# Kernel tuning notes

Measured on AMD Instinct MI355X. Metric: run time of the kernel, lower is better.

Reference implementation:

```python
import jax, jax.numpy as jnp
import numpy as np

B, D_IN, T = 16, 512, 4096
D_CB, K = 8, 1024
COMMITMENT = 1.0


def _weight_norm(v, g):
    # torch weight_norm with dim=0: w[o] = g[o] * v[o] / ||v[o]||
    return g[:, None] * v / jnp.sqrt(jnp.sum(v * v, axis=1, keepdims=True))


def setup_inputs() -> dict:
    key = jax.random.key(0)
    ks = jax.random.split(key, 8)
    return {
        "z": jax.random.normal(ks[0], (B, D_IN, T), dtype=jnp.float32),
        "in_v": jax.random.normal(ks[1], (D_CB, D_IN), dtype=jnp.float32) * 0.05,
        "in_g": jax.random.uniform(ks[2], (D_CB,), dtype=jnp.float32, minval=0.5, maxval=1.5),
        "in_b": jax.random.normal(ks[3], (D_CB,), dtype=jnp.float32) * 0.01,
        "out_v": jax.random.normal(ks[4], (D_IN, D_CB), dtype=jnp.float32) * 0.05,
        "out_g": jax.random.uniform(ks[5], (D_IN,), dtype=jnp.float32, minval=0.5, maxval=1.5),
        "out_b": jax.random.normal(ks[6], (D_IN,), dtype=jnp.float32) * 0.01,
        "codebook": jax.random.normal(ks[7], (K, D_CB), dtype=jnp.float32),
    }


def reference(z, in_v, in_g, in_b, out_v, out_g, out_b, codebook):
    z = z.astype(jnp.float32)
    # in_project: weight-normed 1x1 conv == per-timestep linear [D_IN -> D_CB]
    w_in = _weight_norm(in_v, in_g)                       # [D_CB, D_IN]
    z_e = jnp.einsum('cd,bdt->bct', w_in, z) + in_b[None, :, None]  # [B, D_CB, T]

    enc = jnp.transpose(z_e, (0, 2, 1))                   # [B, T, D_CB]
    cb = codebook.astype(jnp.float32)                     # [K, D_CB]
    # squared euclidean distance via expansion
    d = (jnp.sum(enc * enc, axis=-1, keepdims=True)
         - 2.0 * jnp.einsum('btd,kd->btk', enc, cb)
         + jnp.sum(cb * cb, axis=-1)[None, None, :])      # [B, T, K]
    indices = jnp.argmin(d, axis=-1)                      # [B, T] int

    z_q = jnp.transpose(cb[indices], (0, 2, 1))           # [B, D_CB, T]
    commit_loss = jnp.mean((z_e - jax.lax.stop_gradient(z_q)) ** 2, axis=(1, 2)) * COMMITMENT  # [B]

    # straight-through estimator
    z_q_st = z_e + jax.lax.stop_gradient(z_q - z_e)

    w_out = _weight_norm(out_v, out_g)                    # [D_IN, D_CB]
    out = jnp.einsum('cd,bdt->bct', w_out, z_q_st) + out_b[None, :, None]  # [B, D_IN, T]
    return out, commit_loss, indices
```

## Files before the change

### kernel.cpp

```cpp
#include <hip/hip_runtime.h>
#include <math.h>

#define NB 16
#define DIN 512
#define TT 4096
#define DCB 8
#define KC 1024
#define NW 8


__global__ __launch_bounds__(512) void vq_setup(
    const float* __restrict__ in_v, const float* __restrict__ in_g,
    const float* __restrict__ out_v, const float* __restrict__ out_g,
    const float* __restrict__ cb, float* __restrict__ ws)
{
    int tid = threadIdx.x;
    float* w_inT = ws;
    float* w_out = ws + 4096;
    float* cb2   = ws + 8192;

    {
        int c    = tid >> 6;
        int lane = tid & 63;
        const float* v = in_v + c * DIN;
        float s = 0.f;
        #pragma unroll
        for (int i = 0; i < DIN; i += 64) {
            float x = v[i + lane];
            s += x * x;
        }
        #pragma unroll
        for (int off = 32; off > 0; off >>= 1) s += __shfl_xor(s, off, 64);
        float sq = sqrtf(s);
        float g  = in_g[c];
        #pragma unroll
        for (int i = 0; i < DIN; i += 64) {
            int d = i + lane;
            w_inT[d * DCB + c] = (g * v[d]) / sq;
        }
    }
    {
        int o = tid;
        const float* v = out_v + o * DCB;
        float s = 0.f;
        #pragma unroll
        for (int c = 0; c < DCB; ++c) s += v[c] * v[c];
        float sq = sqrtf(s);
        float g  = out_g[o];
        #pragma unroll
        for (int c = 0; c < DCB; ++c) w_out[o * DCB + c] = (g * v[c]) / sq;
    }
    for (int k = tid; k < KC; k += 512) {
        const float* r = cb + k * DCB;
        float s = 0.f;
        #pragma unroll
        for (int c = 0; c < DCB; ++c) s += r[c] * r[c];
        cb2[k] = s;
    }
}

__global__ __launch_bounds__(512, 4) void vq_main(
    const float* __restrict__ z, const float* __restrict__ in_b,
    const float* __restrict__ out_b, const float* __restrict__ cb,
    const float* __restrict__ ws, float* __restrict__ ws_commit,
    float* __restrict__ out)
{
    __shared__ float s_cb[KC * DCB];
    __shared__ float s_redA[NW * DCB * 64];
    __shared__ float s_redB[NW * DCB * 64];
    __shared__ float s_sdA[NW][64];
    __shared__ int   s_siA[NW][64];
    __shared__ float s_sdB[NW][64];
    __shared__ int   s_siB[NW][64];

    const float* w_inT = ws;
    const float* w_out = ws + 4096;
    const float* cb2w  = ws + 8192;

    int tid  = threadIdx.x;
    int w    = tid >> 6;
    int wu   = __builtin_amdgcn_readfirstlane(w);
    int lane = tid & 63;
    int blk  = blockIdx.x;
    int b    = blk >> 5;
    int p    = blk & 31;
    int tA   = p * 128 + lane;

    {
        float4 c0 = ((const float4*)cb)[tid];
        float4 c1 = ((const float4*)cb)[512 + tid];
        float4 c2 = ((const float4*)cb)[1024 + tid];
        float4 c3 = ((const float4*)cb)[1536 + tid];
        ((float4*)s_cb)[tid]        = c0;
        ((float4*)s_cb)[512 + tid]  = c1;
        ((float4*)s_cb)[1024 + tid] = c2;
        ((float4*)s_cb)[1536 + tid] = c3;
    }

    const float* zpA = z + (size_t)b * DIN * TT + tA;
    int d0 = wu * 64;

    float zeA[DCB];
    #pragma unroll
    for (int c = 0; c < DCB; ++c) zeA[c] = 0.f;
    for (int db = 0; db < 64; db += 8) {
        float v[8];
        #pragma unroll
        for (int j = 0; j < 8; ++j) v[j] = zpA[(size_t)(d0 + db + j) * TT];
        #pragma unroll
        for (int j = 0; j < 8; ++j) {
            const float* wi = w_inT + (d0 + db + j) * DCB;
            #pragma unroll
            for (int c = 0; c < DCB; ++c) zeA[c] = fmaf(wi[c], v[j], zeA[c]);
        }
    }
    {
        float* redw = s_redA + w * (DCB * 64);
        #pragma unroll
        for (int c = 0; c < DCB; ++c) redw[c * 64 + lane] = zeA[c];
    }
    __syncthreads();

    #pragma unroll
    for (int c = 0; c < DCB; ++c) {
        float s = 0.f;
        #pragma unroll
        for (int w2 = 0; w2 < NW; ++w2) s += s_redA[w2 * (DCB * 64) + c * 64 + lane];
        zeA[c] = s + in_b[c];
    }

    float enc2 = 0.f;
    #pragma unroll
    for (int c = 0; c < DCB; ++c) enc2 += zeA[c] * zeA[c];
    {
        float best = 3.4e38f;
        int   bi   = 0;
        int   k0   = wu * 128;
        #pragma unroll 4
        for (int kk = 0; kk < 128; ++kk) {
            int k = k0 + kk;
            float4 r0 = ((const float4*)s_cb)[2 * k];
            float4 r1 = ((const float4*)s_cb)[2 * k + 1];
            float dot = fmaf(zeA[0], r0.x, fmaf(zeA[1], r0.y, fmaf(zeA[2], r0.z, fmaf(zeA[3], r0.w,
                        fmaf(zeA[4], r1.x, fmaf(zeA[5], r1.y, fmaf(zeA[6], r1.z, zeA[7] * r1.w)))))));
            float dk  = (enc2 - 2.0f * dot) + cb2w[k];
            if (dk < best) { best = dk; bi = k; }
        }
        s_sdA[w][lane] = best;
        s_siA[w][lane] = bi;
    }
    __syncthreads();

    float gbest = s_sdA[0][lane];
    int   gbiA  = s_siA[0][lane];
    #pragma unroll
    for (int w2 = 1; w2 < NW; ++w2) {
        float d2 = s_sdA[w2][lane];
        int   i2 = s_siA[w2][lane];
        if (d2 < gbest) { gbest = d2; gbiA = i2; }
    }
    float4 qAa = ((const float4*)s_cb)[2 * gbiA];
    float4 qAb = ((const float4*)s_cb)[2 * gbiA + 1];

    if (wu == 0) {
        float cl = 0.f, f;
        f = zeA[0]-qAa.x; cl = fmaf(f,f,cl);
        f = zeA[1]-qAa.y; cl = fmaf(f,f,cl);
        f = zeA[2]-qAa.z; cl = fmaf(f,f,cl);
        f = zeA[3]-qAa.w; cl = fmaf(f,f,cl);
        f = zeA[4]-qAb.x; cl = fmaf(f,f,cl);
        f = zeA[5]-qAb.y; cl = fmaf(f,f,cl);
        f = zeA[6]-qAb.z; cl = fmaf(f,f,cl);
        f = zeA[7]-qAb.w; cl = fmaf(f,f,cl);
        #pragma unroll
        for (int off = 32; off > 0; off >>= 1) cl += __shfl_xor(cl, off, 64);
        if (lane == 0) ws_commit[b * 64 + 2 * p] = cl;
        out[(size_t)NB * DIN * TT + NB + (size_t)b * TT + tA] = (float)gbiA;
    }

    const float* zpB  = zpA + 64;
    float* outpA = out + (size_t)b * DIN * TT + tA;
    float zeB[DCB];
    #pragma unroll
    for (int c = 0; c < DCB; ++c) zeB[c] = 0.f;
    for (int i = 0; i < 64; i += 4) {
        float v[4];
        #pragma unroll
        for (int j = 0; j < 4; ++j) v[j] = zpB[(size_t)(d0 + i + j) * TT];
        #pragma unroll
        for (int j = 0; j < 4; ++j) {
            int o = d0 + i + j;
            const float* wo = w_out + o * DCB;
            float a = fmaf(wo[0], qAa.x, fmaf(wo[1], qAa.y, fmaf(wo[2], qAa.z, fmaf(wo[3], qAa.w,
                      fmaf(wo[4], qAb.x, fmaf(wo[5], qAb.y, fmaf(wo[6], qAb.z, wo[7] * qAb.w)))))));
            outpA[(size_t)o * TT] = a + out_b[o];
        }
        #pragma unroll
        for (int j = 0; j < 4; ++j) {
            const float* wi = w_inT + (d0 + i + j) * DCB;
            #pragma unroll
            for (int c = 0; c < DCB; ++c) zeB[c] = fmaf(wi[c], v[j], zeB[c]);
        }
    }
    {
        float* redw = s_redB + w * (DCB * 64);
        #pragma unroll
        for (int c = 0; c < DCB; ++c) redw[c * 64 + lane] = zeB[c];
    }
    __syncthreads();

    #pragma unroll
    for (int c = 0; c < DCB; ++c) {
        float s = 0.f;
        #pragma unroll
        for (int w2 = 0; w2 < NW; ++w2) s += s_redB[w2 * (DCB * 64) + c * 64 + lane];
        zeB[c] = s + in_b[c];
    }

    float enc2b = 0.f;
    #pragma unroll
    for (int c = 0; c < DCB; ++c) enc2b += zeB[c] * zeB[c];
    {
        float best = 3.4e38f;
        int   bi   = 0;
        int   k0   = wu * 128;
        #pragma unroll 4
        for (int kk = 0; kk < 128; ++kk) {
            int k = k0 + kk;
            float4 r0 = ((const float4*)s_cb)[2 * k];
            float4 r1 = ((const float4*)s_cb)[2 * k + 1];
            float dot = fmaf(zeB[0], r0.x, fmaf(zeB[1], r0.y, fmaf(zeB[2], r0.z, fmaf(zeB[3], r0.w,
                        fmaf(zeB[4], r1.x, fmaf(zeB[5], r1.y, fmaf(zeB[6], r1.z, zeB[7] * r1.w)))))));
            float dk  = (enc2b - 2.0f * dot) + cb2w[k];
            if (dk < best) { best = dk; bi = k; }
        }
        s_sdB[w][lane] = best;
        s_siB[w][lane] = bi;
    }
    __syncthreads();

    float gbestB = s_sdB[0][lane];
    int   gbiB   = s_siB[0][lane];
    #pragma unroll
    for (int w2 = 1; w2 < NW; ++w2) {
        float d2 = s_sdB[w2][lane];
        int   i2 = s_siB[w2][lane];
        if (d2 < gbestB) { gbestB = d2; gbiB = i2; }
    }
    float4 qBa = ((const float4*)s_cb)[2 * gbiB];
    float4 qBb = ((const float4*)s_cb)[2 * gbiB + 1];

    if (wu == 0) {
        float cl = 0.f, f;
        f = zeB[0]-qBa.x; cl = fmaf(f,f,cl);
        f = zeB[1]-qBa.y; cl = fmaf(f,f,cl);
        f = zeB[2]-qBa.z; cl = fmaf(f,f,cl);
        f = zeB[3]-qBa.w; cl = fmaf(f,f,cl);
        f = zeB[4]-qBb.x; cl = fmaf(f,f,cl);
        f = zeB[5]-qBb.y; cl = fmaf(f,f,cl);
        f = zeB[6]-qBb.z; cl = fmaf(f,f,cl);
        f = zeB[7]-qBb.w; cl = fmaf(f,f,cl);
        #pragma unroll
        for (int off = 32; off > 0; off >>= 1) cl += __shfl_xor(cl, off, 64);
        if (lane == 0) ws_commit[b * 64 + 2 * p + 1] = cl;
        out[(size_t)NB * DIN * TT + NB + (size_t)b * TT + tA + 64] = (float)gbiB;
    }

    float* outpB = outpA + 64;
    #pragma unroll 4
    for (int oo = 0; oo < 64; ++oo) {
        int o = d0 + oo;
        const float* wo = w_out + o * DCB;
        float a = fmaf(wo[0], qBa.x, fmaf(wo[1], qBa.y, fmaf(wo[2], qBa.z, fmaf(wo[3], qBa.w,
                  fmaf(wo[4], qBb.x, fmaf(wo[5], qBb.y, fmaf(wo[6], qBb.z, wo[7] * qBb.w)))))));
        outpB[(size_t)o * TT] = a + out_b[o];
    }
}

__global__ __launch_bounds__(64) void vq_commit(
    const float* __restrict__ ws_commit, float* __restrict__ out)
{
    int b    = blockIdx.x;
    int lane = threadIdx.x;
    float s = ws_commit[b * 64 + lane];
    #pragma unroll
    for (int off = 32; off > 0; off >>= 1) s += __shfl_xor(s, off, 64);
    if (lane == 0)
        out[(size_t)NB * DIN * TT + b] = s * (1.0f / (DCB * TT));
}

extern "C" void kernel_launch(void* const* d_in, const int* in_sizes, int n_in,
                              void* d_out, int out_size, void* d_ws, size_t ws_size,
                              hipStream_t stream) {
    const float* z     = (const float*)d_in[0];
    const float* in_v  = (const float*)d_in[1];
    const float* in_g  = (const float*)d_in[2];
    const float* in_b  = (const float*)d_in[3];
    const float* out_v = (const float*)d_in[4];
    const float* out_g = (const float*)d_in[5];
    const float* out_b = (const float*)d_in[6];
    const float* cb    = (const float*)d_in[7];

    float* ws  = (float*)d_ws;
    float* out = (float*)d_out;

    vq_setup<<<1, 512, 0, stream>>>(in_v, in_g, out_v, out_g, cb, ws);
    vq_main<<<512, 512, 0, stream>>>(z, in_b, out_b, cb, ws, ws + 9216, out);
    vq_commit<<<NB, 64, 0, stream>>>(ws + 9216, out);
}
```

Measured before the change: 76.66 us.

## Interleave codebook scans with projection loads and use packed FP32 distance math

The kernel now overlaps the argmin scan for the first half-tile with the in-projection loads of the second half, and overlaps the second scan with the output-projection stores of the first. The reduction is restructured so each warp finalizes one channel into shared memory. Each lane then scans 64 codes for two timesteps using v_pk_fma_f32 inline assembly, with codebook norms staged in LDS. The commit partials are merged per block. This aims to hide global memory latency behind ALU work and to halve the scan instruction count, at the cost of extra syncs, more LDS and more register pressure.

```diff
diff --git a/kernel.cpp b/kernel.cpp
--- a/kernel.cpp
+++ b/kernel.cpp
@@ -7,6 +7,15 @@
 #define DCB 8
 #define KC 1024
 #define NW 8
+
+typedef float v2f __attribute__((ext_vector_type(2)));
+
+#define PK_MUL_HI(d, a, b)    asm("v_pk_mul_f32 %0, %1, %2 op_sel:[0,1]"          : "=v"(d) : "v"(a), "v"(b))
+#define PK_FMA_LO(d, a, b, c) asm("v_pk_fma_f32 %0, %1, %2, %3 op_sel_hi:[1,0,1]" : "=v"(d) : "v"(a), "v"(b), "v"(c))
+#define PK_FMA_HI(d, a, b, c) asm("v_pk_fma_f32 %0, %1, %2, %3 op_sel:[0,1,0]"    : "=v"(d) : "v"(a), "v"(b), "v"(c))
+#define PK_FMA(d, a, b, c)    asm("v_pk_fma_f32 %0, %1, %2, %3"                   : "=v"(d) : "v"(a), "v"(b), "v"(c))
+#define PK_ADD_LO(d, a, b)    asm("v_pk_add_f32 %0, %1, %2 op_sel_hi:[1,0]"       : "=v"(d) : "v"(a), "v"(b))
+#define PK_ADD_HI(d, a, b)    asm("v_pk_add_f32 %0, %1, %2 op_sel:[0,1]"          : "=v"(d) : "v"(a), "v"(b))
 
 
 __global__ __launch_bounds__(512) void vq_setup(
@@ -59,6 +68,39 @@
     }
 }
 
+__device__ __forceinline__ void scan2(const float* s_cb, const float* s_cb2,
+    int kbase, const v2f* zt, v2f enc2p,
+    float& best0, float& best1, int& bi0, int& bi1)
+{
+    v2f c2q = *(const v2f*)(s_cb2 + kbase);
+    #pragma unroll
+    for (int u = 0; u < 2; ++u) {
+        int k = kbase + u;
+        float4 r0 = ((const float4*)s_cb)[2 * k];
+        float4 r1 = ((const float4*)s_cb)[2 * k + 1];
+        v2f cbA = (v2f){r0.x, r0.y};
+        v2f cbB = (v2f){r0.z, r0.w};
+        v2f cbC = (v2f){r1.x, r1.y};
+        v2f cbD = (v2f){r1.z, r1.w};
+        v2f acc;
+        PK_MUL_HI(acc, zt[7], cbD);
+        PK_FMA_LO(acc, zt[6], cbD, acc);
+        PK_FMA_HI(acc, zt[5], cbC, acc);
+        PK_FMA_LO(acc, zt[4], cbC, acc);
+        PK_FMA_HI(acc, zt[3], cbB, acc);
+        PK_FMA_LO(acc, zt[2], cbB, acc);
+        PK_FMA_HI(acc, zt[1], cbA, acc);
+        PK_FMA_LO(acc, zt[0], cbA, acc);
+        v2f neg2 = (v2f){-2.0f, -2.0f};
+        v2f dk2;
+        PK_FMA(dk2, acc, neg2, enc2p);
+        if (u == 0) { PK_ADD_LO(dk2, dk2, c2q); }
+        else        { PK_ADD_HI(dk2, dk2, c2q); }
+        if (dk2.x < best0) { best0 = dk2.x; bi0 = k; }
+        if (dk2.y < best1) { best1 = dk2.y; bi1 = k; }
+    }
+}
+
 __global__ __launch_bounds__(512, 4) void vq_main(
     const float* __restrict__ z, const float* __restrict__ in_b,
     const float* __restrict__ out_b, const float* __restrict__ cb,
@@ -66,16 +108,15 @@
     float* __restrict__ out)
 {
     __shared__ float s_cb[KC * DCB];
-    __shared__ float s_redA[NW * DCB * 64];
-    __shared__ float s_redB[NW * DCB * 64];
-    __shared__ float s_sdA[NW][64];
-    __shared__ int   s_siA[NW][64];
-    __shared__ float s_sdB[NW][64];
-    __shared__ int   s_siB[NW][64];
+    __shared__ float s_cb2[KC];
+    __shared__ float s_red[NW * DCB * 64];
+    __shared__ float s_zeA[DCB * 64];
+    __shared__ float s_zeB[DCB * 64];
+    __shared__ float s_sd[16][64];
+    __shared__ int   s_si[16][64];
 
     const float* w_inT = ws;
     const float* w_out = ws + 4096;
-    const float* cb2w  = ws + 8192;
 
     int tid  = threadIdx.x;
     int w    = tid >> 6;
@@ -83,8 +124,8 @@
     int lane = tid & 63;
     int blk  = blockIdx.x;
     int b    = blk >> 5;
-    int p    = blk & 31;
-    int tA   = p * 128 + lane;
+    int t0   = (blk & 31) * 128;
+    int d0   = wu * 64;
 
     {
         float4 c0 = ((const float4*)cb)[tid];
@@ -95,10 +136,13 @@
         ((float4*)s_cb)[512 + tid]  = c1;
         ((float4*)s_cb)[1024 + tid] = c2;
         ((float4*)s_cb)[1536 + tid] = c3;
-    }
-
-    const float* zpA = z + (size_t)b * DIN * TT + tA;
-    int d0 = wu * 64;
+        if (tid < 256) {
+            float4 q = ((const float4*)(ws + 8192))[tid];
+            ((float4*)s_cb2)[tid] = q;
+        }
+    }
+
+    const float* zpA = z + (size_t)b * DIN * TT + t0 + lane;
 
     float zeA[DCB];
     #pragma unroll
@@ -114,156 +158,158 @@
             for (int c = 0; c < DCB; ++c) zeA[c] = fmaf(wi[c], v[j], zeA[c]);
         }
     }
-    {
-        float* redw = s_redA + w * (DCB * 64);
-        #pragma unroll
-        for (int c = 0; c < DCB; ++c) redw[c * 64 + lane] = zeA[c];
-    }
-    __syncthreads();
-
-    #pragma unroll
-    for (int c = 0; c < DCB; ++c) {
-        float s = 0.f;
-        #pragma unroll
-        for (int w2 = 0; w2 < NW; ++w2) s += s_redA[w2 * (DCB * 64) + c * 64 + lane];
-        zeA[c] = s + in_b[c];
-    }
-
-    float enc2 = 0.f;
-    #pragma unroll
-    for (int c = 0; c < DCB; ++c) enc2 += zeA[c] * zeA[c];
-    {
-        float best = 3.4e38f;
-        int   bi   = 0;
-        int   k0   = wu * 128;
-        #pragma unroll 4
-        for (int kk = 0; kk < 128; ++kk) {
-            int k = k0 + kk;
-            float4 r0 = ((const float4*)s_cb)[2 * k];
-            float4 r1 = ((const float4*)s_cb)[2 * k + 1];
-            float dot = fmaf(zeA[0], r0.x, fmaf(zeA[1], r0.y, fmaf(zeA[2], r0.z, fmaf(zeA[3], r0.w,
-                        fmaf(zeA[4], r1.x, fmaf(zeA[5], r1.y, fmaf(zeA[6], r1.z, zeA[7] * r1.w)))))));
-            float dk  = (enc2 - 2.0f * dot) + cb2w[k];
-            if (dk < best) { best = dk; bi = k; }
-        }
-        s_sdA[w][lane] = best;
-        s_siA[w][lane] = bi;
-    }
-    __syncthreads();
-
-    float gbest = s_sdA[0][lane];
-    int   gbiA  = s_siA[0][lane];
-    #pragma unroll
-    for (int w2 = 1; w2 < NW; ++w2) {
-        float d2 = s_sdA[w2][lane];
-        int   i2 = s_siA[w2][lane];
-        if (d2 < gbest) { gbest = d2; gbiA = i2; }
+    #pragma unroll
+    for (int c = 0; c < DCB; ++c) s_red[w * 512 + c * 64 + lane] = zeA[c];
+    __syncthreads();
+
+    {
+        float sa = 0.f;
+        #pragma unroll
+        for (int w2 = 0; w2 < NW; ++w2) sa += s_red[w2 * 512 + w * 64 + lane];
+        s_zeA[w * 64 + lane] = sa + in_b[w];
+    }
+    __syncthreads();
+
+    int h    = lane >> 5;
+    int t2   = 2 * (lane & 31);
+    int sidx = 2 * w + h;
+    int k0   = 64 * sidx;
+
+    v2f zA[DCB];
+    #pragma unroll
+    for (int c = 0; c < DCB; ++c) zA[c] = *(const v2f*)(s_zeA + c * 64 + t2);
+    v2f enc2pA;
+    {
+        float e0 = 0.f, e1 = 0.f;
+        #pragma unroll
+        for (int c = 0; c < DCB; ++c) { e0 += zA[c].x * zA[c].x; e1 += zA[c].y * zA[c].y; }
+        enc2pA = (v2f){e0, e1};
+    }
+    float bestA0 = 3.4e38f, bestA1 = 3.4e38f;
+    int   biA0 = 0, biA1 = 0;
+
+    const float* zpB = zpA + 64;
+    float zeB[DCB];
+    #pragma unroll
+    for (int c = 0; c < DCB; ++c) zeB[c] = 0.f;
+    for (int it = 0; it < 8; ++it) {
+        float v[8];
+        #pragma unroll
+        for (int j = 0; j < 8; ++j)
+            v[j] = zpB[(size_t)(d0 + it * 8 + j) * TT];
+        #pragma unroll
+        for (int kk = 0; kk < 8; kk += 2)
+            scan2(s_cb, s_cb2, k0 + it * 8 + kk, zA, enc2pA, bestA0, bestA1, biA0, biA1);
+        #pragma unroll
+        for (int j = 0; j < 8; ++j) {
+            const float* wi = w_inT + (d0 + it * 8 + j) * DCB;
+            #pragma unroll
+            for (int c = 0; c < DCB; ++c) zeB[c] = fmaf(wi[c], v[j], zeB[c]);
+        }
+    }
+    #pragma unroll
+    for (int c = 0; c < DCB; ++c) s_red[w * 512 + c * 64 + lane] = zeB[c];
+    *(float2*)(&s_sd[sidx][t2]) = make_float2(bestA0, bestA1);
+    *(int2*)  (&s_si[sidx][t2]) = make_int2(biA0, biA1);
+    __syncthreads();
+
+    int gbiA;
+    {
+        float g = s_sd[0][lane];
+        gbiA = s_si[0][lane];
+        #pragma unroll
+        for (int s2 = 1; s2 < 16; ++s2) {
+            float d2 = s_sd[s2][lane];
+            int   i2 = s_si[s2][lane];
+            if (d2 < g) { g = d2; gbiA = i2; }
+        }
     }
     float4 qAa = ((const float4*)s_cb)[2 * gbiA];
     float4 qAb = ((const float4*)s_cb)[2 * gbiA + 1];
 
+    {
+        float sa = 0.f;
+        #pragma unroll
+        for (int w2 = 0; w2 < NW; ++w2) sa += s_red[w2 * 512 + w * 64 + lane];
+        s_zeB[w * 64 + lane] = sa + in_b[w];
+    }
+    __syncthreads();
+
+    float clA = 0.f;
     if (wu == 0) {
-        float cl = 0.f, f;
-        f = zeA[0]-qAa.x; cl = fmaf(f,f,cl);
-        f = zeA[1]-qAa.y; cl = fmaf(f,f,cl);
-        f = zeA[2]-qAa.z; cl = fmaf(f,f,cl);
-        f = zeA[3]-qAa.w; cl = fmaf(f,f,cl);
-        f = zeA[4]-qAb.x; cl = fmaf(f,f,cl);
-        f = zeA[5]-qAb.y; cl = fmaf(f,f,cl);
-        f = zeA[6]-qAb.z; cl = fmaf(f,f,cl);
-        f = zeA[7]-qAb.w; cl = fmaf(f,f,cl);
-        #pragma unroll
-        for (int off = 32; off > 0; off >>= 1) cl += __shfl_xor(cl, off, 64);
-        if (lane == 0) ws_commit[b * 64 + 2 * p] = cl;
-        out[(size_t)NB * DIN * TT + NB + (size_t)b * TT + tA] = (float)gbiA;
-    }
-
-    const float* zpB  = zpA + 64;
-    float* outpA = out + (size_t)b * DIN * TT + tA;
-    float zeB[DCB];
-    #pragma unroll
-    for (int c = 0; c < DCB; ++c) zeB[c] = 0.f;
-    for (int i = 0; i < 64; i += 4) {
-        float v[4];
-        #pragma unroll
-        for (int j = 0; j < 4; ++j) v[j] = zpB[(size_t)(d0 + i + j) * TT];
-        #pragma unroll
-        for (int j = 0; j < 4; ++j) {
-            int o = d0 + i + j;
+        float f;
+        f = s_zeA[0*64+lane]-qAa.x; clA = fmaf(f,f,clA);
+        f = s_zeA[1*64+lane]-qAa.y; clA = fmaf(f,f,clA);
+        f = s_zeA[2*64+lane]-qAa.z; clA = fmaf(f,f,clA);
+        f = s_zeA[3*64+lane]-qAa.w; clA = fmaf(f,f,clA);
+        f = s_zeA[4*64+lane]-qAb.x; clA = fmaf(f,f,clA);
+        f = s_zeA[5*64+lane]-qAb.y; clA = fmaf(f,f,clA);
+        f = s_zeA[6*64+lane]-qAb.z; clA = fmaf(f,f,clA);
+        f = s_zeA[7*64+lane]-qAb.w; clA = fmaf(f,f,clA);
+        #pragma unroll
+        for (int off = 32; off > 0; off >>= 1) clA += __shfl_xor(clA, off, 64);
+        out[(size_t)NB * DIN * TT + NB + (size_t)b * TT + t0 + lane] = (float)gbiA;
+    }
+
+    v2f zB[DCB];
+    #pragma unroll
+    for (int c = 0; c < DCB; ++c) zB[c] = *(const v2f*)(s_zeB + c * 64 + t2);
+    v2f enc2pB;
+    {
+        float e0 = 0.f, e1 = 0.f;
+        #pragma unroll
+        for (int c = 0; c < DCB; ++c) { e0 += zB[c].x * zB[c].x; e1 += zB[c].y * zB[c].y; }
+        enc2pB = (v2f){e0, e1};
+    }
+    float bestB0 = 3.4e38f, bestB1 = 3.4e38f;
+    int   biB0 = 0, biB1 = 0;
+
+    float* outpA = out + (size_t)b * DIN * TT + t0 + lane;
+    for (int it = 0; it < 8; ++it) {
+        #pragma unroll
+        for (int j = 0; j < 8; ++j) {
+            int o = d0 + it * 8 + j;
             const float* wo = w_out + o * DCB;
             float a = fmaf(wo[0], qAa.x, fmaf(wo[1], qAa.y, fmaf(wo[2], qAa.z, fmaf(wo[3], qAa.w,
                       fmaf(wo[4], qAb.x, fmaf(wo[5], qAb.y, fmaf(wo[6], qAb.z, wo[7] * qAb.w)))))));
             outpA[(size_t)o * TT] = a + out_b[o];
         }
         #pragma unroll
-        for (int j = 0; j < 4; ++j) {
-            const float* wi = w_inT + (d0 + i + j) * DCB;
-            #pragma unroll
-            for (int c = 0; c < DCB; ++c) zeB[c] = fmaf(wi[c], v[j], zeB[c]);
-        }
-    }
-    {
-        float* redw = s_redB + w * (DCB * 64);
-        #pragma unroll
-        for (int c = 0; c < DCB; ++c) redw[c * 64 + lane] = zeB[c];
-    }
-    __syncthreads();
-
-    #pragma unroll
-    for (int c = 0; c < DCB; ++c) {
-        float s = 0.f;
-        #pragma unroll
-        for (int w2 = 0; w2 < NW; ++w2) s += s_redB[w2 * (DCB * 64) + c * 64 + lane];
-        zeB[c] = s + in_b[c];
-    }
-
-    float enc2b = 0.f;
-    #pragma unroll
-    for (int c = 0; c < DCB; ++c) enc2b += zeB[c] * zeB[c];
-    {
-        float best = 3.4e38f;
-        int   bi   = 0;
-        int   k0   = wu * 128;
-        #pragma unroll 4
-        for (int kk = 0; kk < 128; ++kk) {
-            int k = k0 + kk;
-            float4 r0 = ((const float4*)s_cb)[2 * k];
-            float4 r1 = ((const float4*)s_cb)[2 * k + 1];
-            float dot = fmaf(zeB[0], r0.x, fmaf(zeB[1], r0.y, fmaf(zeB[2], r0.z, fmaf(zeB[3], r0.w,
-                        fmaf(zeB[4], r1.x, fmaf(zeB[5], r1.y, fmaf(zeB[6], r1.z, zeB[7] * r1.w)))))));
-            float dk  = (enc2b - 2.0f * dot) + cb2w[k];
-            if (dk < best) { best = dk; bi = k; }
-        }
-        s_sdB[w][lane] = best;
-        s_siB[w][lane] = bi;
-    }
-    __syncthreads();
-
-    float gbestB = s_sdB[0][lane];
-    int   gbiB   = s_siB[0][lane];
-    #pragma unroll
-    for (int w2 = 1; w2 < NW; ++w2) {
-        float d2 = s_sdB[w2][lane];
-        int   i2 = s_siB[w2][lane];
-        if (d2 < gbestB) { gbestB = d2; gbiB = i2; }
+        for (int kk = 0; kk < 8; kk += 2)
+            scan2(s_cb, s_cb2, k0 + it * 8 + kk, zB, enc2pB, bestB0, bestB1, biB0, biB1);
+    }
+    *(float2*)(&s_sd[sidx][t2]) = make_float2(bestB0, bestB1);
+    *(int2*)  (&s_si[sidx][t2]) = make_int2(biB0, biB1);
+    __syncthreads();
+
+    int gbiB;
+    {
+        float g = s_sd[0][lane];
+        gbiB = s_si[0][lane];
+        #pragma unroll
+        for (int s2 = 1; s2 < 16; ++s2) {
+            float d2 = s_sd[s2][lane];
+            int   i2 = s_si[s2][lane];
+            if (d2 < g) { g = d2; gbiB = i2; }
+        }
     }
     float4 qBa = ((const float4*)s_cb)[2 * gbiB];
     float4 qBb = ((const float4*)s_cb)[2 * gbiB + 1];
 
     if (wu == 0) {
-        float cl = 0.f, f;
-        f = zeB[0]-qBa.x; cl = fmaf(f,f,cl);
-        f = zeB[1]-qBa.y; cl = fmaf(f,f,cl);
-        f = zeB[2]-qBa.z; cl = fmaf(f,f,cl);
-        f = zeB[3]-qBa.w; cl = fmaf(f,f,cl);
-        f = zeB[4]-qBb.x; cl = fmaf(f,f,cl);
-        f = zeB[5]-qBb.y; cl = fmaf(f,f,cl);
-        f = zeB[6]-qBb.z; cl = fmaf(f,f,cl);
-        f = zeB[7]-qBb.w; cl = fmaf(f,f,cl);
-        #pragma unroll
-        for (int off = 32; off > 0; off >>= 1) cl += __shfl_xor(cl, off, 64);
-        if (lane == 0) ws_commit[b * 64 + 2 * p + 1] = cl;
-        out[(size_t)NB * DIN * TT + NB + (size_t)b * TT + tA + 64] = (float)gbiB;
+        float clB = 0.f, f;
+        f = s_zeB[0*64+lane]-qBa.x; clB = fmaf(f,f,clB);
+        f = s_zeB[1*64+lane]-qBa.y; clB = fmaf(f,f,clB);
+        f = s_zeB[2*64+lane]-qBa.z; clB = fmaf(f,f,clB);
+        f = s_zeB[3*64+lane]-qBa.w; clB = fmaf(f,f,clB);
+        f = s_zeB[4*64+lane]-qBb.x; clB = fmaf(f,f,clB);
+        f = s_zeB[5*64+lane]-qBb.y; clB = fmaf(f,f,clB);
+        f = s_zeB[6*64+lane]-qBb.z; clB = fmaf(f,f,clB);
+        f = s_zeB[7*64+lane]-qBb.w; clB = fmaf(f,f,clB);
+        #pragma unroll
+        for (int off = 32; off > 0; off >>= 1) clB += __shfl_xor(clB, off, 64);
+        if (lane == 0) ws_commit[blk] = clA + clB;
+        out[(size_t)NB * DIN * TT + NB + (size_t)b * TT + t0 + 64 + lane] = (float)gbiB;
     }
 
     float* outpB = outpA + 64;
@@ -282,7 +328,7 @@
 {
     int b    = blockIdx.x;
     int lane = threadIdx.x;
-    float s = ws_commit[b * 64 + lane];
+    float s = (lane < 32) ? ws_commit[b * 32 + lane] : 0.f;
     #pragma unroll
     for (int off = 32; off > 0; off >>= 1) s += __shfl_xor(s, off, 64);
     if (lane == 0)
```

Measured after the change: 72.52 us. -5.4%, faster.
